# Kernel tuning notes

Hardware: AMD Instinct MI355X
Metric: run time of the kernel (lower is better)

The kernel has to match this reference:

```python
import jax, jax.numpy as jnp
import numpy as np

V = 32000   # vocab_size
L = 4       # n_layer
H = 12      # n_head
C = 768     # n_embd
T = 1024    # block_size / seq len
B = 4       # batch
D = C // H  # head_dim
F = 4 * C   # mlp hidden


def setup_inputs() -> dict:
    key = jax.random.key(0)
    ks = jax.random.split(key, 12)
    n = lambda k, sh: (jax.random.normal(k, sh, dtype=jnp.float32) * 0.02)
    return {
        "idx": jax.random.randint(ks[0], (B, T), 0, V, dtype=jnp.int32),
        "tok_emb": n(ks[1], (V, C)),
        "pos_emb": n(ks[2], (T, C)),
        "Wq": n(ks[3], (L, C, C)),
        "Wk": n(ks[4], (L, C, C)),
        "Wv": n(ks[5], (L, C, C)),
        "Wp": n(ks[6], (L, C, C)),
        "bp": jnp.zeros((L, C), jnp.float32),
        "ln1s": jnp.ones((L, C), jnp.float32),
        "ln1b": jnp.zeros((L, C), jnp.float32),
        "ln2s": jnp.ones((L, C), jnp.float32),
        "ln2b": jnp.zeros((L, C), jnp.float32),
        "W1": n(ks[7], (L, C, F)),
        "b1": jnp.zeros((L, F), jnp.float32),
        "W2": n(ks[8], (L, F, C)),
        "b2": jnp.zeros((L, C), jnp.float32),
        "lnfs": jnp.ones((C,), jnp.float32),
        "lnfb": jnp.zeros((C,), jnp.float32),
        "Whead": n(ks[9], (C, V)),
    }


def _ln(x, s, b):
    m = x.mean(-1, keepdims=True)
    v = ((x - m) ** 2).mean(-1, keepdims=True)
    return (x - m) * jax.lax.rsqrt(v + 1e-5) * s + b


def reference(idx, tok_emb, pos_emb, Wq, Wk, Wv, Wp, bp, ln1s, ln1b, ln2s, ln2b,
              W1, b1, W2, b2, lnfs, lnfb, Whead):
    Bc, Tc = idx.shape
    x = tok_emb[idx] + pos_emb[None, :Tc]               # [B,T,C]
    mask = jnp.tril(jnp.ones((Tc, Tc), bool))           # causal mask
    scale = 1.0 / np.sqrt(D)
    for l in range(L):
        # --- causal self-attention (explicit QK^T, masked softmax) ---
        h = _ln(x, ln1s[l], ln1b[l])
        q = (h @ Wq[l]).reshape(Bc, Tc, H, D).transpose(0, 2, 1, 3)  # [B,H,T,D]
        k = (h @ Wk[l]).reshape(Bc, Tc, H, D).transpose(0, 2, 1, 3)
        v = (h @ Wv[l]).reshape(Bc, Tc, H, D).transpose(0, 2, 1, 3)
        att = jnp.einsum('bhqd,bhkd->bhqk', q, k) * scale            # [B,H,T,T]
        att = jnp.where(mask, att, -jnp.inf)
        att = jax.nn.softmax(att, axis=-1)
        y = jnp.einsum('bhqk,bhkd->bhqd', att, v)
        y = y.transpose(0, 2, 1, 3).reshape(Bc, Tc, C)
        x = x + (y @ Wp[l] + bp[l])
        # --- GELU MLP ---
        h = _ln(x, ln2s[l], ln2b[l])
        x = x + (jax.nn.gelu(h @ W1[l] + b1[l], approximate=False) @ W2[l] + b2[l])
    x = _ln(x, lnfs, lnfb)
    logits = x @ Whead                                  # [B,T,V]
    return logits
```

## Files before the change

### kernel.cpp

```cpp
#include <hip/hip_runtime.h>
#include <stdint.h>

#define B_ 4
#define T_ 1024
#define C_ 768
#define H_ 12
#define D_ 64
#define F_ 3072
#define V_ 32000
#define L_ 4

typedef unsigned short ushort_t;
typedef __bf16 bf16x8 __attribute__((ext_vector_type(8)));
typedef float f32x4 __attribute__((ext_vector_type(4)));
typedef unsigned short u16x8 __attribute__((ext_vector_type(8)));

__device__ __forceinline__ float b2f(unsigned short u) {
    union { unsigned int i; float f; } x; x.i = ((unsigned int)u) << 16; return x.f;
}
__device__ __forceinline__ unsigned short f2b(float f) {
    union { float f; unsigned int i; } x; x.f = f;
    unsigned int r = x.i + 0x7FFFu + ((x.i >> 16) & 1u);
    return (unsigned short)(r >> 16);
}

__device__ __forceinline__ float gelu_f(float u) {
    float z = fabsf(u) * 0.70710678118654752f;
    float t = __builtin_amdgcn_rcpf(1.0f + 0.3275911f * z);
    float poly = t * (0.254829592f + t * (-0.284496736f + t * (1.421413741f +
                 t * (-1.453152027f + t * 1.061405429f))));
    float erfz = 1.0f - poly * __expf(-z * z);
    return u * 0.5f * (1.0f + copysignf(erfz, u));
}

__device__ __forceinline__ void gload16(const ushort_t* g, ushort_t* l) {
    __builtin_amdgcn_global_load_lds(
        (const __attribute__((address_space(1))) unsigned int*)g,
        (__attribute__((address_space(3))) unsigned int*)l, 16, 0, 0);
}

__global__ __launch_bounds__(256) void k_embed(const int* __restrict__ idx,
        const float* __restrict__ tok, const float* __restrict__ pos,
        float* __restrict__ x) {
    int i = blockIdx.x * 256 + threadIdx.x;
    int m = i / (C_ / 4);
    int cc = (i % (C_ / 4)) * 4;
    int t = m & (T_ - 1);
    int tokid = idx[m];
    float4 te = *(const float4*)&tok[(size_t)tokid * C_ + cc];
    float4 pe = *(const float4*)&pos[(size_t)t * C_ + cc];
    *(float4*)&x[(size_t)m * C_ + cc] =
        make_float4(te.x + pe.x, te.y + pe.y, te.z + pe.z, te.w + pe.w);
}

__global__ __launch_bounds__(256) void k_ln(const float* __restrict__ x,
        const float* __restrict__ s, const float* __restrict__ b,
        ushort_t* __restrict__ out) {
    const int lane = threadIdx.x & 63, wave = threadIdx.x >> 6;
    const int row = blockIdx.x * 4 + wave;
    const float* xr = x + (size_t)row * C_;
    float4 v[3];
    float sum = 0.f, sq = 0.f;
#pragma unroll
    for (int j = 0; j < 3; ++j) {
        v[j] = *(const float4*)&xr[lane * 4 + j * 256];
        sum += v[j].x + v[j].y + v[j].z + v[j].w;
        sq  += v[j].x * v[j].x + v[j].y * v[j].y + v[j].z * v[j].z + v[j].w * v[j].w;
    }
#pragma unroll
    for (int off = 1; off < 64; off <<= 1) {
        sum += __shfl_xor(sum, off);
        sq  += __shfl_xor(sq,  off);
    }
    float mean = sum * (1.f / C_);
    float var  = sq * (1.f / C_) - mean * mean;
    float rstd = rsqrtf(var + 1e-5f);
#pragma unroll
    for (int j = 0; j < 3; ++j) {
        int c = lane * 4 + j * 256;
        float4 sv = *(const float4*)&s[c];
        float4 bv = *(const float4*)&b[c];
        ushort4 o;
        o.x = f2b((v[j].x - mean) * rstd * sv.x + bv.x);
        o.y = f2b((v[j].y - mean) * rstd * sv.y + bv.y);
        o.z = f2b((v[j].z - mean) * rstd * sv.z + bv.z);
        o.w = f2b((v[j].w - mean) * rstd * sv.w + bv.w);
        *(ushort4*)&out[(size_t)row * C_ + c] = o;
    }
}

__global__ void k_tcvt(const float* __restrict__ in, ushort_t* __restrict__ out,
                       int R, int C) {
    __shared__ float tile[32][33];
    const float* src = in + (size_t)blockIdx.z * R * C;
    ushort_t* dst = out + (size_t)blockIdx.z * R * C;
    int r0 = blockIdx.y * 32, c0 = blockIdx.x * 32;
    int tx = threadIdx.x, ty = threadIdx.y;
#pragma unroll
    for (int i = ty; i < 32; i += 8)
        tile[i][tx] = src[(size_t)(r0 + i) * C + c0 + tx];
    __syncthreads();
#pragma unroll
    for (int i = ty; i < 32; i += 8)
        dst[(size_t)(c0 + i) * R + r0 + tx] = f2b(tile[tx][i]);
}

__global__ void k_tcvt16(const float* __restrict__ wq, const float* __restrict__ wk,
                         const float* __restrict__ wv, const float* __restrict__ wp,
                         ushort_t* __restrict__ out) {
    __shared__ float tile[32][33];
    int l = blockIdx.z >> 2, w = blockIdx.z & 3;
    const float* src = (w == 0 ? wq : w == 1 ? wk : w == 2 ? wv : wp) + (size_t)l * C_ * C_;
    ushort_t* dst = out + (size_t)blockIdx.z * C_ * C_;
    int r0 = blockIdx.y * 32, c0 = blockIdx.x * 32;
    int tx = threadIdx.x, ty = threadIdx.y;
#pragma unroll
    for (int i = ty; i < 32; i += 8)
        tile[i][tx] = src[(size_t)(r0 + i) * C_ + c0 + tx];
    __syncthreads();
#pragma unroll
    for (int i = ty; i < 32; i += 8)
        dst[(size_t)(c0 + i) * C_ + r0 + tx] = f2b(tile[tx][i]);
}

template <int EPI>
__global__ __launch_bounds__(256) void k_gemm(
        const ushort_t* __restrict__ A, const ushort_t* __restrict__ BT,
        const float* __restrict__ bias, const float* __restrict__ resid,
        float* __restrict__ outf, ushort_t* __restrict__ outb,
        ushort_t* __restrict__ outb2, ushort_t* __restrict__ outb3,
        int M, int N, int K) {
    __shared__ __align__(16) ushort_t S[24576];
    const int tid = threadIdx.x;
    const int lane = tid & 63, wave = tid >> 6;
    const int lr = lane & 15, lg = lane >> 4;
    const int wm = (wave >> 1) * 64, wn = (wave & 1) * 64;

    const int bid = blockIdx.x;
    const int m_in = bid & 7;
    const int strip = (bid >> 3) & 3;
    const int ncol = bid >> 5;
    const int m0 = (strip * 8 + m_in) << 7;
    const int n0 = ncol << 7;

    const int sr = wave * 16 + (lane >> 2);
    const int sc = (((lane & 3) ^ ((lane >> 3) & 3)) << 3);

    f32x4 acc[4][4];
#pragma unroll
    for (int i = 0; i < 4; ++i)
#pragma unroll
        for (int j = 0; j < 4; ++j) acc[i][j] = (f32x4){0.f, 0.f, 0.f, 0.f};

    auto stage = [&](int k0, int buf) {
        ushort_t* as = S + buf * 4096;
        ushort_t* bs = S + 12288 + buf * 4096;
        gload16(&A [(size_t)(m0 + sr)      * K + k0 + sc], as + (wave * 16) * 32);
        gload16(&A [(size_t)(m0 + 64 + sr) * K + k0 + sc], as + (64 + wave * 16) * 32);
        gload16(&BT[(size_t)(n0 + sr)      * K + k0 + sc], bs + (wave * 16) * 32);
        gload16(&BT[(size_t)(n0 + 64 + sr) * K + k0 + sc], bs + (64 + wave * 16) * 32);
    };

    const int nt = K >> 5;
    stage(0, 0);
    stage(32, 1);
    int cur = 0, pre = 2;
    const int swzr = (lr >> 1) & 3;
    for (int t = 0; t < nt; ++t) {
        if (t + 1 < nt) asm volatile("s_waitcnt vmcnt(4)" ::: "memory");
        else            asm volatile("s_waitcnt vmcnt(0)" ::: "memory");
        __builtin_amdgcn_sched_barrier(0);
        __builtin_amdgcn_s_barrier();
        const ushort_t* as = S + cur * 4096;
        const ushort_t* bs = S + 12288 + cur * 4096;
        bf16x8 af[4], bfr[4];
#pragma unroll
        for (int i = 0; i < 4; ++i)
            af[i]  = *(const bf16x8*)&as[(wm + i * 16 + lr) * 32 + ((lg ^ swzr) << 3)];
#pragma unroll
        for (int j = 0; j < 4; ++j)
            bfr[j] = *(const bf16x8*)&bs[(wn + j * 16 + lr) * 32 + ((lg ^ swzr) << 3)];
        if (t + 2 < nt) stage((t + 2) << 5, pre);
#pragma unroll
        for (int i = 0; i < 4; ++i)
#pragma unroll
            for (int j = 0; j < 4; ++j)
                acc[i][j] = __builtin_amdgcn_mfma_f32_16x16x32_bf16(af[i], bfr[j], acc[i][j], 0, 0, 0);
        cur = (cur == 2) ? 0 : cur + 1;
        pre = (pre == 2) ? 0 : pre + 1;
    }

    if (EPI == 0 || EPI == 2) {
        float* cls = (float*)S;
#pragma unroll
        for (int h = 0; h < 2; ++h) {
            __syncthreads();
            if ((wm >> 6) == h) {
#pragma unroll
                for (int i = 0; i < 4; ++i)
#pragma unroll
                    for (int j = 0; j < 4; ++j)
#pragma unroll
                        for (int r = 0; r < 4; ++r)
                            cls[(i * 16 + lg * 4 + r) * 128 + wn + j * 16 + lr] = acc[i][j][r];
            }
            __syncthreads();
#pragma unroll
            for (int p = 0; p < 8; ++p) {
                int row = p * 8 + (tid >> 5);
                int colc = (tid & 31) * 4;
                f32x4 val = *(const f32x4*)&cls[row * 128 + colc];
                size_t gidx = (size_t)(m0 + h * 64 + row) * N + n0 + colc;
                if (EPI == 2) {
                    f32x4 rv = *(const f32x4*)&resid[gidx];
                    f32x4 bv = *(const f32x4*)&bias[n0 + colc];
                    val = val + rv + bv;
                    *(f32x4*)&outf[gidx] = val;
                } else {
                    __builtin_nontemporal_store(val, (f32x4*)&outf[gidx]);
                }
            }
        }
        return;
    }

    if (EPI == 1) {
        ushort_t* cls = S;
        __syncthreads();
#pragma unroll
        for (int i = 0; i < 4; ++i)
#pragma unroll
            for (int j = 0; j < 4; ++j) {
                float bval = bias[n0 + wn + j * 16 + lr];
#pragma unroll
                for (int r = 0; r < 4; ++r)
                    cls[(wm + i * 16 + lg * 4 + r) * 128 + wn + j * 16 + lr] =
                        f2b(gelu_f(acc[i][j][r] + bval));
            }
        __syncthreads();
#pragma unroll
        for (int p = 0; p < 8; ++p) {
            int row = p * 16 + (tid >> 4);
            int colc = (tid & 15) * 8;
            u16x8 val = *(const u16x8*)&cls[row * 128 + colc];
            *(u16x8*)&outb[(size_t)(m0 + row) * N + n0 + colc] = val;
        }
        return;
    }

#pragma unroll
    for (int i = 0; i < 4; ++i) {
#pragma unroll
        for (int j = 0; j < 4; ++j) {
            int col = n0 + wn + j * 16 + lr;
#pragma unroll
            for (int r = 0; r < 4; ++r) {
                int row = m0 + wm + i * 16 + lg * 4 + r;
                float v = acc[i][j][r];
                int nm = col / 768, c = col % 768;
                int hh = c >> 6, d = c & 63;
                int bb = row >> 10, t = row & 1023;
                ushort_t val = f2b(v);
                if (nm == 0)
                    outb [((((size_t)bb * H_ + hh) << 10) + t) * D_ + d] = val;
                else if (nm == 1)
                    outb2[((((size_t)bb * H_ + hh) << 10) + t) * D_ + d] = val;
                else
                    outb3[(((size_t)bb * H_ + hh) * D_ + d) * T_ + t] = val;
            }
        }
    }
}

__global__ __launch_bounds__(256) void k_attn(const ushort_t* __restrict__ q,
        const ushort_t* __restrict__ k, const ushort_t* __restrict__ vT,
        ushort_t* __restrict__ yc) {
    __shared__ __align__(16) ushort_t P[4][16 * 64];
    const int lane = threadIdx.x & 63, wave = threadIdx.x >> 6;
    const int lr = lane & 15, lg = lane >> 4;
    const int bh = blockIdx.x;
    const int bb = bh / H_, hh = bh % H_;
    const int qrow0 = (gridDim.y - 1 - blockIdx.y) * 64 + wave * 16;
    const ushort_t* qb = q + (size_t)bh * T_ * D_;
    const ushort_t* kb = k + (size_t)bh * T_ * D_;
    const ushort_t* vb = vT + (size_t)bh * D_ * T_;

    bf16x8 aq0 = *(const bf16x8*)&qb[(qrow0 + lr) * D_ + lg * 8];
    bf16x8 aq1 = *(const bf16x8*)&qb[(qrow0 + lr) * D_ + 32 + lg * 8];

    f32x4 accY[4];
    float ls[4];
#pragma unroll
    for (int d = 0; d < 4; ++d) accY[d] = (f32x4){0.f, 0.f, 0.f, 0.f};
#pragma unroll
    for (int r = 0; r < 4; ++r) ls[r] = 0.f;

    ushort_t* pw = &P[wave][0];
    const int kv_end = qrow0 + 16;
    for (int kv0 = 0; kv0 < kv_end; kv0 += 64) {
        f32x4 s[4];
#pragma unroll
        for (int j = 0; j < 4; ++j) s[j] = (f32x4){0.f, 0.f, 0.f, 0.f};
        __builtin_amdgcn_s_setprio(1);
#pragma unroll
        for (int j = 0; j < 4; ++j) {
            bf16x8 bk0 = *(const bf16x8*)&kb[(kv0 + j * 16 + lr) * D_ + lg * 8];
            bf16x8 bk1 = *(const bf16x8*)&kb[(kv0 + j * 16 + lr) * D_ + 32 + lg * 8];
            s[j] = __builtin_amdgcn_mfma_f32_16x16x32_bf16(aq0, bk0, s[j], 0, 0, 0);
            s[j] = __builtin_amdgcn_mfma_f32_16x16x32_bf16(aq1, bk1, s[j], 0, 0, 0);
        }
        __builtin_amdgcn_s_setprio(0);

        const bool full = (kv0 + 63 <= qrow0);
        float p[4][4];
#pragma unroll
        for (int r = 0; r < 4; ++r) {
            int row = qrow0 + lg * 4 + r;
            float ps = 0.f;
            if (full) {
#pragma unroll
                for (int j = 0; j < 4; ++j) { p[j][r] = __expf(s[j][r] * 0.125f); ps += p[j][r]; }
            } else {
#pragma unroll
                for (int j = 0; j < 4; ++j) {
                    int col = kv0 + j * 16 + lr;
                    float a = (col <= row) ? s[j][r] * 0.125f : -1e30f;
                    p[j][r] = __expf(a); ps += p[j][r];
                }
            }
            ps += __shfl_xor(ps, 1);
            ps += __shfl_xor(ps, 2);
            ps += __shfl_xor(ps, 4);
            ps += __shfl_xor(ps, 8);
            ls[r] += ps;
        }

        asm volatile("s_waitcnt lgkmcnt(0)" ::: "memory");
        __builtin_amdgcn_sched_barrier(0);
#pragma unroll
        for (int r = 0; r < 4; ++r)
#pragma unroll
            for (int j = 0; j < 4; ++j)
                pw[(lg * 4 + r) * 64 + j * 16 + lr] = f2b(p[j][r]);
        asm volatile("s_waitcnt lgkmcnt(0)" ::: "memory");
        __builtin_amdgcn_sched_barrier(0);
        bf16x8 pa0 = *(const bf16x8*)&pw[lr * 64 + lg * 8];
        bf16x8 pa1 = *(const bf16x8*)&pw[lr * 64 + 32 + lg * 8];
        __builtin_amdgcn_s_setprio(1);
#pragma unroll
        for (int d = 0; d < 4; ++d) {
            bf16x8 bv0 = *(const bf16x8*)&vb[(d * 16 + lr) * T_ + kv0 + lg * 8];
            bf16x8 bv1 = *(const bf16x8*)&vb[(d * 16 + lr) * T_ + kv0 + 32 + lg * 8];
            accY[d] = __builtin_amdgcn_mfma_f32_16x16x32_bf16(pa0, bv0, accY[d], 0, 0, 0);
            accY[d] = __builtin_amdgcn_mfma_f32_16x16x32_bf16(pa1, bv1, accY[d], 0, 0, 0);
        }
        __builtin_amdgcn_s_setprio(0);
    }
    float inv[4];
#pragma unroll
    for (int r = 0; r < 4; ++r) inv[r] = 1.0f / ls[r];
#pragma unroll
    for (int d = 0; d < 4; ++d)
#pragma unroll
        for (int r = 0; r < 4; ++r) {
            int row = qrow0 + lg * 4 + r;
            yc[((size_t)bb * T_ + row) * C_ + hh * D_ + d * 16 + lr] = f2b(accY[d][r] * inv[r]);
        }
}

extern "C" void kernel_launch(void* const* d_in, const int* in_sizes, int n_in,
                              void* d_out, int out_size, void* d_ws, size_t ws_size,
                              hipStream_t stream) {
    (void)in_sizes; (void)n_in; (void)out_size; (void)ws_size;
    const int*   idx  = (const int*)d_in[0];
    const float* tok  = (const float*)d_in[1];
    const float* pos  = (const float*)d_in[2];
    const float* Wq   = (const float*)d_in[3];
    const float* Wk   = (const float*)d_in[4];
    const float* Wv   = (const float*)d_in[5];
    const float* Wp   = (const float*)d_in[6];
    const float* bp   = (const float*)d_in[7];
    const float* ln1s = (const float*)d_in[8];
    const float* ln1b = (const float*)d_in[9];
    const float* ln2s = (const float*)d_in[10];
    const float* ln2b = (const float*)d_in[11];
    const float* W1   = (const float*)d_in[12];
    const float* b1   = (const float*)d_in[13];
    const float* W2   = (const float*)d_in[14];
    const float* b2   = (const float*)d_in[15];
    const float* lnfs = (const float*)d_in[16];
    const float* lnfb = (const float*)d_in[17];
    const float* Wh   = (const float*)d_in[18];
    float* out = (float*)d_out;

    char* ws = (char*)d_ws;
    size_t off = 0;
    auto alloc = [&](size_t bytes) { void* p = ws + off; off += (bytes + 255) & ~(size_t)255; return p; };

    const size_t CCE = (size_t)C_ * C_;
    const size_t CFE = (size_t)C_ * F_;
    ushort_t* wCC  = (ushort_t*)alloc(16 * CCE * 2);
    ushort_t* w1T  = (ushort_t*)alloc((size_t)L_ * CFE * 2);
    ushort_t* w2T  = (ushort_t*)alloc((size_t)L_ * CFE * 2);
    ushort_t* whT  = (ushort_t*)alloc((size_t)C_ * V_ * 2);
    float*    x    = (float*)   alloc((size_t)B_ * T_ * C_ * 4);
    ushort_t* h    = (ushort_t*)alloc((size_t)B_ * T_ * C_ * 2);
    ushort_t* qb_  = (ushort_t*)alloc((size_t)B_ * T_ * C_ * 2);
    ushort_t* kb_  = (ushort_t*)alloc((size_t)B_ * T_ * C_ * 2);
    ushort_t* vTb  = (ushort_t*)alloc((size_t)B_ * T_ * C_ * 2);
    ushort_t* yc   = (ushort_t*)alloc((size_t)B_ * T_ * C_ * 2);
    ushort_t* mh   = (ushort_t*)alloc((size_t)B_ * T_ * F_ * 2);

    dim3 tb(32, 8);
    k_tcvt16<<<dim3(24, 24, 16), tb, 0, stream>>>(Wq, Wk, Wv, Wp, wCC);
    k_tcvt<<<dim3(96, 24, 4), tb, 0, stream>>>(W1, w1T, C_, F_);
    k_tcvt<<<dim3(24, 96, 4), tb, 0, stream>>>(W2, w2T, F_, C_);
    k_tcvt<<<dim3(1000, 24, 1), tb, 0, stream>>>(Wh, whT, C_, V_);

    k_embed<<<3072, 256, 0, stream>>>(idx, tok, pos, x);

    for (int l = 0; l < L_; ++l) {
        k_ln<<<1024, 256, 0, stream>>>(x, ln1s + l * C_, ln1b + l * C_, h);
        k_gemm<3><<<18 * 32, 256, 0, stream>>>(h, wCC + (size_t)(l * 4) * CCE,
            nullptr, nullptr, nullptr, qb_, kb_, vTb, 4096, 3 * C_, C_);
        k_attn<<<dim3(48, 16), 256, 0, stream>>>(qb_, kb_, vTb, yc);
        k_gemm<2><<<6 * 32, 256, 0, stream>>>(yc, wCC + (size_t)(l * 4 + 3) * CCE,
            bp + l * C_, x, x, nullptr, nullptr, nullptr, 4096, C_, C_);
        k_ln<<<1024, 256, 0, stream>>>(x, ln2s + l * C_, ln2b + l * C_, h);
        k_gemm<1><<<24 * 32, 256, 0, stream>>>(h, w1T + (size_t)l * CFE,
            b1 + l * F_, nullptr, nullptr, mh, nullptr, nullptr, 4096, F_, C_);
        k_gemm<2><<<6 * 32, 256, 0, stream>>>(mh, w2T + (size_t)l * CFE,
            b2 + l * C_, x, x, nullptr, nullptr, nullptr, 4096, C_, F_);
    }
    k_ln<<<1024, 256, 0, stream>>>(x, lnfs, lnfb, h);
    k_gemm<0><<<250 * 32, 256, 0, stream>>>(h, whT, nullptr, nullptr,
        out, nullptr, nullptr, nullptr, 4096, V_, C_);
}
```

Measured before the change: 1.098 ms.

## Add 256x256-tile GEMM kernel for LM head projection

Adds a dedicated 512-thread GEMM kernel with 256x256 output tiles, K-step 64, double-buffered LDS staging, swizzled loads and raised wave priority around the MFMA blocks. It is used for the final vocabulary projection in place of the generic 128x128 GEMM. The larger tile raises arithmetic intensity and cuts redundant A/B loads for the largest GEMM in the program. The cost is heavier register and LDS use per block, which lowers occupancy. The generic kernel's EPI==0 path is removed as now unused.

Result: no change. 1.110 ms (+1.1%).

```diff
diff --git a/kernel.cpp b/kernel.cpp
--- a/kernel.cpp
+++ b/kernel.cpp
@@ -190,7 +190,7 @@
         pre = (pre == 2) ? 0 : pre + 1;
     }
 
-    if (EPI == 0 || EPI == 2) {
+    if (EPI == 2) {
         float* cls = (float*)S;
 #pragma unroll
         for (int h = 0; h < 2; ++h) {
@@ -211,14 +211,10 @@
                 int colc = (tid & 31) * 4;
                 f32x4 val = *(const f32x4*)&cls[row * 128 + colc];
                 size_t gidx = (size_t)(m0 + h * 64 + row) * N + n0 + colc;
-                if (EPI == 2) {
-                    f32x4 rv = *(const f32x4*)&resid[gidx];
-                    f32x4 bv = *(const f32x4*)&bias[n0 + colc];
-                    val = val + rv + bv;
-                    *(f32x4*)&outf[gidx] = val;
-                } else {
-                    __builtin_nontemporal_store(val, (f32x4*)&outf[gidx]);
-                }
+                f32x4 rv = *(const f32x4*)&resid[gidx];
+                f32x4 bv = *(const f32x4*)&bias[n0 + colc];
+                val = val + rv + bv;
+                *(f32x4*)&outf[gidx] = val;
             }
         }
         return;
@@ -268,6 +264,115 @@
                 else
                     outb3[(((size_t)bb * H_ + hh) * D_ + d) * T_ + t] = val;
             }
+        }
+    }
+}
+
+__global__ __launch_bounds__(512, 2) void k_gemm256(
+        const ushort_t* __restrict__ A, const ushort_t* __restrict__ BT,
+        float* __restrict__ outf, int M, int N, int K) {
+    __shared__ __align__(16) ushort_t S[65536];
+    const int tid = threadIdx.x;
+    const int lane = tid & 63, wave = tid >> 6;
+    const int lr = lane & 15, lg = lane >> 4;
+    const int wm = (wave >> 2) * 128, wn = (wave & 3) * 64;
+
+    const int bid = blockIdx.x;
+    const int m_in = bid & 7;
+    const int strip = (bid >> 3) & 1;
+    const int ncol = bid >> 4;
+    const int m0 = (strip * 8 + m_in) << 8;
+    const int n0 = ncol << 8;
+
+    const int rofs = lane >> 3;
+    const int cch = ((lane & 7) ^ ((lane >> 3) & 7)) << 3;
+
+    f32x4 acc[8][4];
+#pragma unroll
+    for (int i = 0; i < 8; ++i)
+#pragma unroll
+        for (int j = 0; j < 4; ++j) acc[i][j] = (f32x4){0.f, 0.f, 0.f, 0.f};
+
+    auto stage = [&](int k0, int buf) {
+#pragma unroll
+        for (int q = 0; q < 4; ++q) {
+            int rbase = (wave * 4 + q) * 8;
+            gload16(&A[(size_t)(m0 + rbase + rofs) * K + k0 + cch],
+                    S + buf * 16384 + rbase * 64);
+        }
+#pragma unroll
+        for (int q = 0; q < 4; ++q) {
+            int rbase = (wave * 4 + q) * 8;
+            gload16(&BT[(size_t)(n0 + rbase + rofs) * K + k0 + cch],
+                    S + 32768 + buf * 16384 + rbase * 64);
+        }
+    };
+
+    const int nt = K >> 6;
+    stage(0, 0);
+    stage(64, 1);
+    const int rsw = lr & 7;
+    for (int t = 0; t < nt; ++t) {
+        if (t + 1 < nt) asm volatile("s_waitcnt vmcnt(8)" ::: "memory");
+        else            asm volatile("s_waitcnt vmcnt(0)" ::: "memory");
+        __builtin_amdgcn_sched_barrier(0);
+        __builtin_amdgcn_s_barrier();
+        const ushort_t* ab = S + (t & 1) * 16384;
+        const ushort_t* bb = S + 32768 + (t & 1) * 16384;
+#pragma unroll
+        for (int kki = 0; kki < 2; ++kki) {
+            const int kc = kki * 4;
+            bf16x8 bfr[4];
+#pragma unroll
+            for (int j = 0; j < 4; ++j)
+                bfr[j] = *(const bf16x8*)&bb[(wn + j * 16 + lr) * 64 + (((kc + lg) ^ rsw) << 3)];
+#pragma unroll
+            for (int half = 0; half < 2; ++half) {
+                bf16x8 af[4];
+#pragma unroll
+                for (int i2 = 0; i2 < 4; ++i2)
+                    af[i2] = *(const bf16x8*)&ab[(wm + (half * 4 + i2) * 16 + lr) * 64 +
+                                                 (((kc + lg) ^ rsw) << 3)];
+                asm volatile("s_waitcnt lgkmcnt(0)" ::: "memory");
+                __builtin_amdgcn_sched_barrier(0);
+                __builtin_amdgcn_s_setprio(1);
+#pragma unroll
+                for (int i2 = 0; i2 < 4; ++i2)
+#pragma unroll
+                    for (int j = 0; j < 4; ++j)
+                        acc[half * 4 + i2][j] = __builtin_amdgcn_mfma_f32_16x16x32_bf16(
+                            af[i2], bfr[j], acc[half * 4 + i2][j], 0, 0, 0);
+                __builtin_amdgcn_s_setprio(0);
+            }
+        }
+        __builtin_amdgcn_s_barrier();
+        if (t + 2 < nt) stage((t + 2) << 6, t & 1);
+    }
+
+    float* cls = (float*)S;
+#pragma unroll
+    for (int h = 0; h < 4; ++h) {
+        __syncthreads();
+        if ((wave >> 2) == (h >> 1)) {
+            const int ibase = (h & 1) * 4;
+#pragma unroll
+            for (int i2 = 0; i2 < 4; ++i2)
+#pragma unroll
+                for (int j = 0; j < 4; ++j)
+#pragma unroll
+                    for (int r = 0; r < 4; ++r)
+                        cls[(i2 * 16 + lg * 4 + r) * 260 + wn + j * 16 + lr] =
+                            acc[ibase + i2][j][r];
+        }
+        __syncthreads();
+#pragma unroll
+        for (int p = 0; p < 8; ++p) {
+            int idx = p * 512 + tid;
+            int row = idx >> 6;
+            int colc = (idx & 63) * 4;
+            f32x4 val = *(const f32x4*)&cls[row * 260 + colc];
+            __builtin_nontemporal_store(val,
+                (f32x4*)&outf[(size_t)(m0 + h * 64 + row) * N + n0 + colc]);
         }
     }
 }
@@ -433,6 +538,5 @@
             b2 + l * C_, x, x, nullptr, nullptr, nullptr, 4096, C_, F_);
     }
     k_ln<<<1024, 256, 0, stream>>>(x, lnfs, lnfb, h);
-    k_gemm<0><<<250 * 32, 256, 0, stream>>>(h, whT, nullptr, nullptr,
-        out, nullptr, nullptr, nullptr, 4096, V_, C_);
-}
+    k_gemm256<<<2000, 512, 0, stream>>>(h, whT, out, 4096, V_, C_);
+}
```

## Widen attention KV tile to 128 and transpose score MFMA for row-local sums

Applied to the files above, without the earlier changes.

The attention kernel now processes 128 keys per iteration instead of 64. It computes S^T by swapping the MFMA operands, so each lane holds one query row's scores. That turns the per-row softmax sum into a cheaper two-step cross-group shuffle, and the P tile can be written to padded shared memory with 4-wide vector stores. This halves loop iterations and shuffle reductions per key, at the cost of more registers and more masked work on the diagonal tile.

Result: no change. 1.091 ms (-0.7%).

```diff
diff --git a/kernel.cpp b/kernel.cpp
--- a/kernel.cpp
+++ b/kernel.cpp
@@ -275,7 +275,7 @@
 __global__ __launch_bounds__(256) void k_attn(const ushort_t* __restrict__ q,
         const ushort_t* __restrict__ k, const ushort_t* __restrict__ vT,
         ushort_t* __restrict__ yc) {
-    __shared__ __align__(16) ushort_t P[4][16 * 64];
+    __shared__ __align__(16) ushort_t P[4][16 * 136];
     const int lane = threadIdx.x & 63, wave = threadIdx.x >> 6;
     const int lr = lane & 15, lg = lane >> 4;
     const int bh = blockIdx.x;
@@ -289,76 +289,70 @@
     bf16x8 aq1 = *(const bf16x8*)&qb[(qrow0 + lr) * D_ + 32 + lg * 8];
 
     f32x4 accY[4];
-    float ls[4];
+    float ls = 0.f;
 #pragma unroll
     for (int d = 0; d < 4; ++d) accY[d] = (f32x4){0.f, 0.f, 0.f, 0.f};
-#pragma unroll
-    for (int r = 0; r < 4; ++r) ls[r] = 0.f;
 
     ushort_t* pw = &P[wave][0];
     const int kv_end = qrow0 + 16;
-    for (int kv0 = 0; kv0 < kv_end; kv0 += 64) {
-        f32x4 s[4];
-#pragma unroll
-        for (int j = 0; j < 4; ++j) s[j] = (f32x4){0.f, 0.f, 0.f, 0.f};
-        __builtin_amdgcn_s_setprio(1);
-#pragma unroll
-        for (int j = 0; j < 4; ++j) {
+    for (int kv0 = 0; kv0 < kv_end; kv0 += 128) {
+        const bool full = (kv0 + 127 <= qrow0);
+        float p[8][4];
+        float ps = 0.f;
+#pragma unroll
+        for (int j = 0; j < 8; ++j) {
+            f32x4 s = (f32x4){0.f, 0.f, 0.f, 0.f};
             bf16x8 bk0 = *(const bf16x8*)&kb[(kv0 + j * 16 + lr) * D_ + lg * 8];
             bf16x8 bk1 = *(const bf16x8*)&kb[(kv0 + j * 16 + lr) * D_ + 32 + lg * 8];
-            s[j] = __builtin_amdgcn_mfma_f32_16x16x32_bf16(aq0, bk0, s[j], 0, 0, 0);
-            s[j] = __builtin_amdgcn_mfma_f32_16x16x32_bf16(aq1, bk1, s[j], 0, 0, 0);
-        }
-        __builtin_amdgcn_s_setprio(0);
-
-        const bool full = (kv0 + 63 <= qrow0);
-        float p[4][4];
-#pragma unroll
-        for (int r = 0; r < 4; ++r) {
-            int row = qrow0 + lg * 4 + r;
-            float ps = 0.f;
+            __builtin_amdgcn_s_setprio(1);
+            s = __builtin_amdgcn_mfma_f32_16x16x32_bf16(bk0, aq0, s, 0, 0, 0);
+            s = __builtin_amdgcn_mfma_f32_16x16x32_bf16(bk1, aq1, s, 0, 0, 0);
+            __builtin_amdgcn_s_setprio(0);
             if (full) {
 #pragma unroll
-                for (int j = 0; j < 4; ++j) { p[j][r] = __expf(s[j][r] * 0.125f); ps += p[j][r]; }
+                for (int r = 0; r < 4; ++r) { p[j][r] = __expf(s[r] * 0.125f); ps += p[j][r]; }
             } else {
-#pragma unroll
-                for (int j = 0; j < 4; ++j) {
-                    int col = kv0 + j * 16 + lr;
-                    float a = (col <= row) ? s[j][r] * 0.125f : -1e30f;
-                    p[j][r] = __expf(a); ps += p[j][r];
+                int kcb = kv0 + j * 16 + lg * 4;
+#pragma unroll
+                for (int r = 0; r < 4; ++r) {
+                    p[j][r] = (kcb + r <= qrow0 + lr) ? __expf(s[r] * 0.125f) : 0.f;
+                    ps += p[j][r];
                 }
             }
-            ps += __shfl_xor(ps, 1);
-            ps += __shfl_xor(ps, 2);
-            ps += __shfl_xor(ps, 4);
-            ps += __shfl_xor(ps, 8);
-            ls[r] += ps;
-        }
+        }
+        ps += __shfl_xor(ps, 16);
+        ps += __shfl_xor(ps, 32);
+        ls += ps;
 
         asm volatile("s_waitcnt lgkmcnt(0)" ::: "memory");
         __builtin_amdgcn_sched_barrier(0);
 #pragma unroll
-        for (int r = 0; r < 4; ++r)
-#pragma unroll
-            for (int j = 0; j < 4; ++j)
-                pw[(lg * 4 + r) * 64 + j * 16 + lr] = f2b(p[j][r]);
+        for (int j = 0; j < 8; ++j) {
+            ushort4 w;
+            w.x = f2b(p[j][0]); w.y = f2b(p[j][1]);
+            w.z = f2b(p[j][2]); w.w = f2b(p[j][3]);
+            *(ushort4*)&pw[lr * 136 + j * 16 + lg * 4] = w;
+        }
         asm volatile("s_waitcnt lgkmcnt(0)" ::: "memory");
         __builtin_amdgcn_sched_barrier(0);
-        bf16x8 pa0 = *(const bf16x8*)&pw[lr * 64 + lg * 8];
-        bf16x8 pa1 = *(const bf16x8*)&pw[lr * 64 + 32 + lg * 8];
-        __builtin_amdgcn_s_setprio(1);
+        bf16x8 pa[4];
+#pragma unroll
+        for (int ks = 0; ks < 4; ++ks)
+            pa[ks] = *(const bf16x8*)&pw[lr * 136 + ks * 32 + lg * 8];
 #pragma unroll
         for (int d = 0; d < 4; ++d) {
-            bf16x8 bv0 = *(const bf16x8*)&vb[(d * 16 + lr) * T_ + kv0 + lg * 8];
-            bf16x8 bv1 = *(const bf16x8*)&vb[(d * 16 + lr) * T_ + kv0 + 32 + lg * 8];
-            accY[d] = __builtin_amdgcn_mfma_f32_16x16x32_bf16(pa0, bv0, accY[d], 0, 0, 0);
-            accY[d] = __builtin_amdgcn_mfma_f32_16x16x32_bf16(pa1, bv1, accY[d], 0, 0, 0);
-        }
-        __builtin_amdgcn_s_setprio(0);
+            __builtin_amdgcn_s_setprio(1);
+#pragma unroll
+            for (int ks = 0; ks < 4; ++ks) {
+                bf16x8 bv = *(const bf16x8*)&vb[(d * 16 + lr) * T_ + kv0 + ks * 32 + lg * 8];
+                accY[d] = __builtin_amdgcn_mfma_f32_16x16x32_bf16(pa[ks], bv, accY[d], 0, 0, 0);
+            }
+            __builtin_amdgcn_s_setprio(0);
+        }
     }
     float inv[4];
 #pragma unroll
-    for (int r = 0; r < 4; ++r) inv[r] = 1.0f / ls[r];
+    for (int r = 0; r < 4; ++r) inv[r] = 1.0f / __shfl(ls, lg * 4 + r);
 #pragma unroll
     for (int d = 0; d < 4; ++d)
 #pragma unroll
```
